# Performance work log

Hardware: AMD Instinct MI355X
Metric: run time of the kernel (lower is better)

The kernel has to match this reference:

```python
import jax, jax.numpy as jnp
import numpy as np

T = 64      # simulation_length
B = 128     # batch
D = 2048    # flattened input dim / axons per core
N = 2048    # neurons per core
L = 4       # number of cores (chain, latency = index)
OUT = 1024  # number of output_sources


def setup_inputs() -> dict:
    key = jax.random.key(0)
    k0, k1, k2, k3 = jax.random.split(key, 4)
    x = jax.random.uniform(k0, (B, D), dtype=jnp.float32)          # rate-coded input in [0,1)
    # core_params[l] = core_matrix.transpose() -> shape [N, A]; scaled for sane membrane dynamics
    W = jax.random.normal(k1, (L, N, D), dtype=jnp.float32) * 0.05
    thresholds = jnp.ones((L,), dtype=jnp.float32)
    # axon_sources: per-core irregular gather indices into previous core's neurons (input for l=0)
    axon_idx = jax.random.randint(k2, (L, D), 0, D, dtype=jnp.int32)
    out_idx = jax.random.randint(k3, (OUT,), 0, N, dtype=jnp.int32)
    return dict(x=x, W=W, thresholds=thresholds, axon_idx=axon_idx,
                out_idx=out_idx, simulation_length=T)


def _ideal_spike_scan(avg, thr, T):
    """Per-cycle: m += avg; spike = (m > thr); m[m > thr] -= thr.  avg: [B, N]."""
    def step(m, _):
        m = m + avg
        s = (m > thr).astype(m.dtype)
        return m - thr * s, s
    _, spikes = jax.lax.scan(step, jnp.zeros_like(avg), None, length=T)
    return spikes  # [T, B, N]


def reference(x, W, thresholds, axon_idx, out_idx, simulation_length):
    T = simulation_length
    L = W.shape[0]
    # generate_input_spike_train: x replicated across all cycles -> cache[-1]
    prev = jnp.broadcast_to(x, (T,) + x.shape)  # [T, B, D]
    for l in range(L):
        # get_signal_tensor: gather axon source signals for every cycle
        gathered = prev[:, :, axon_idx[l]]                    # [T, B, A]
        # per-cycle matmul: torch.matmul(core_params, sig.T).T == sig @ W[l].T
        val = jnp.einsum('tba,na->tbn', gathered, W[l])       # [T, B, N]
        avg = val.mean(axis=0)                                # avg_values [B, N]
        # ideal membrane integrate + threshold-reset recurrence -> out spike train
        prev = _ideal_spike_scan(avg, thresholds[l], T)       # [T, B, N]
    # output_signals: sum of output-source spikes over all cycles
    return prev[:, :, out_idx].sum(axis=0)                    # [B, OUT]
```

## Files before the change

kernel.cpp:

```cpp
#include <hip/hip_runtime.h>

#define BB   128
#define DD   2048
#define NN   2048
#define LL   4
#define OUTN 1024
#define JBQ  32

typedef double double4v __attribute__((ext_vector_type(4)));

__global__ __launch_bounds__(256) void gather0_kernel(
    const float* __restrict__ x, const int* __restrict__ idx0,
    float* __restrict__ At)
{
    int i = blockIdx.x * 256 + threadIdx.x;
    int k = i >> 7;
    int b = i & 127;
    At[i] = x[b * DD + idx0[k]];
}

__global__ __launch_bounds__(256, 2) void layer_kernel(
    const float* __restrict__ srcT,
    const int*   __restrict__ idx,
    const float* __restrict__ Wl,
    const float* __restrict__ thresholds, int l,
    const int*   __restrict__ Tptr,
    float* __restrict__ dst, int isLast)
{
    __shared__ double red[4 * 64 * 8];

    const int t    = threadIdx.x;
    const int wq   = t >> 6;
    const int lane = t & 63;
    const int q    = lane >> 4;
    const int c    = lane & 15;

    const int g     = blockIdx.x;
    const int btile = (g >> 3) & 7;
    const int nsup  = (g & 7) | ((g >> 6) << 3);
    const int n0    = nsup * 32;
    const int bcol  = btile * 16 + c;

    double4v pr = {0., 0., 0., 0.}, pcv = {0., 0., 0., 0.};
    pr  = __builtin_amdgcn_mfma_f64_16x16x4f64(0.25 * (double)c, 1.0, pr, 0, 0, 0);
    pcv = __builtin_amdgcn_mfma_f64_16x16x4f64(0.25, (double)c, pcv, 0, 0, 0);
    int rowD[4], colD[4];
    #pragma unroll
    for (int r = 0; r < 4; ++r) {
        rowD[r] = (int)(pr[r] + 0.25);
        colD[r] = (int)(pcv[r] + 0.25);
    }

    double4v acc0[4] = {{0.,0.,0.,0.},{0.,0.,0.,0.},{0.,0.,0.,0.},{0.,0.,0.,0.}};
    double4v acc1[4] = {{0.,0.,0.,0.},{0.,0.,0.,0.},{0.,0.,0.,0.},{0.,0.,0.,0.}};

    const int    kbase = wq * (DD / 4);
    const float* wb0   = Wl + (size_t)(n0 + c) * DD + kbase + 4 * q;
    const float* wb1   = wb0 + (size_t)16 * DD;
    const int*   ibase = idx ? (idx + kbase + 4 * q) : nullptr;

    float4 wv0[4], wv1[4];
    float4 sv[4];
    int4   iv[4];

    #pragma unroll
    for (int p = 0; p < 4; ++p) {
        wv0[p] = *(const float4*)(wb0 + 16 * p);
        wv1[p] = *(const float4*)(wb1 + 16 * p);
    }
    #pragma unroll
    for (int p = 0; p < 4; ++p) {
        int r0, r1, r2, r3;
        if (ibase) {
            int4 iv0 = *(const int4*)(ibase + 16 * p);
            r0 = iv0.x; r1 = iv0.y; r2 = iv0.z; r3 = iv0.w;
        } else {
            int kb = kbase + 16 * p + 4 * q;
            r0 = kb; r1 = kb + 1; r2 = kb + 2; r3 = kb + 3;
        }
        sv[p].x = srcT[(size_t)r0 * BB + bcol];
        sv[p].y = srcT[(size_t)r1 * BB + bcol];
        sv[p].z = srcT[(size_t)r2 * BB + bcol];
        sv[p].w = srcT[(size_t)r3 * BB + bcol];
    }
    if (ibase) {
        #pragma unroll
        for (int p = 0; p < 4; ++p) iv[p] = *(const int4*)(ibase + 16 * (4 + p));
    }

    for (int u = 0; u < JBQ / 4; ++u) {
        #pragma unroll
        for (int gg = 0; gg < 4; ++gg) {
            float4 w0 = wv0[gg];
            float4 w1 = wv1[gg];
            float4 s  = sv[gg];

            int jn = 4 * u + 4 + gg; if (jn > JBQ - 1) jn = JBQ - 1;
            wv0[gg] = *(const float4*)(wb0 + 16 * jn);
            wv1[gg] = *(const float4*)(wb1 + 16 * jn);

            int r0, r1, r2, r3;
            if (ibase) {
                int4 ivv = iv[gg];
                r0 = ivv.x; r1 = ivv.y; r2 = ivv.z; r3 = ivv.w;
            } else {
                int kb = kbase + 16 * jn + 4 * q;
                r0 = kb; r1 = kb + 1; r2 = kb + 2; r3 = kb + 3;
            }
            sv[gg].x = srcT[(size_t)r0 * BB + bcol];
            sv[gg].y = srcT[(size_t)r1 * BB + bcol];
            sv[gg].z = srcT[(size_t)r2 * BB + bcol];
            sv[gg].w = srcT[(size_t)r3 * BB + bcol];

            if (ibase) {
                int jm = 4 * u + 8 + gg; if (jm > JBQ - 1) jm = JBQ - 1;
                iv[gg] = *(const int4*)(ibase + 16 * jm);
            }

            acc0[0] = __builtin_amdgcn_mfma_f64_16x16x4f64((double)w0.x, (double)s.x, acc0[0], 0, 0, 0);
            acc1[0] = __builtin_amdgcn_mfma_f64_16x16x4f64((double)w1.x, (double)s.x, acc1[0], 0, 0, 0);
            acc0[1] = __builtin_amdgcn_mfma_f64_16x16x4f64((double)w0.y, (double)s.y, acc0[1], 0, 0, 0);
            acc1[1] = __builtin_amdgcn_mfma_f64_16x16x4f64((double)w1.y, (double)s.y, acc1[1], 0, 0, 0);
            acc0[2] = __builtin_amdgcn_mfma_f64_16x16x4f64((double)w0.z, (double)s.z, acc0[2], 0, 0, 0);
            acc1[2] = __builtin_amdgcn_mfma_f64_16x16x4f64((double)w1.z, (double)s.z, acc1[2], 0, 0, 0);
            acc0[3] = __builtin_amdgcn_mfma_f64_16x16x4f64((double)w0.w, (double)s.w, acc0[3], 0, 0, 0);
            acc1[3] = __builtin_amdgcn_mfma_f64_16x16x4f64((double)w1.w, (double)s.w, acc1[3], 0, 0, 0);
        }
    }

    double4v a0 = (acc0[0] + acc0[1]) + (acc0[2] + acc0[3]);
    double4v a1 = (acc1[0] + acc1[1]) + (acc1[2] + acc1[3]);

    {
        double* my = red + ((size_t)wq * 64 + lane) * 8;
        #pragma unroll
        for (int r = 0; r < 4; ++r) { my[r] = a0[r]; my[4 + r] = a1[r]; }
    }
    __syncthreads();
    if (wq < 2) {
        const int off = wq * 4;
        double a[4];
        #pragma unroll
        for (int r = 0; r < 4; ++r) {
            a[r] =  red[((size_t)0 * 64 + lane) * 8 + off + r];
            a[r] += red[((size_t)1 * 64 + lane) * 8 + off + r];
            a[r] += red[((size_t)2 * 64 + lane) * 8 + off + r];
            a[r] += red[((size_t)3 * 64 + lane) * 8 + off + r];
        }

        const double th = (double)thresholds[l];
        const int T = *Tptr;
        const float sc = isLast ? 1.0f : (1.0f / (float)T);
        double m0 = 0., m1 = 0., m2 = 0., m3 = 0.;
        int c0 = 0, c1 = 0, c2 = 0, c3 = 0;
        for (int tt = 0; tt < T; ++tt) {
            m0 += a[0]; if (m0 > th) { c0++; m0 -= th; }
            m1 += a[1]; if (m1 > th) { c1++; m1 -= th; }
            m2 += a[2]; if (m2 > th) { c2++; m2 -= th; }
            m3 += a[3]; if (m3 > th) { c3++; m3 -= th; }
        }
        int cnt[4] = {c0, c1, c2, c3};
        #pragma unroll
        for (int r = 0; r < 4; ++r) {
            int n = n0 + 16 * wq + rowD[r];
            dst[(size_t)n * BB + btile * 16 + colD[r]] = (float)cnt[r] * sc;
        }
    }
}

__global__ __launch_bounds__(256) void out_kernel(
    const float* __restrict__ cntT, const int* __restrict__ out_idx,
    float* __restrict__ out)
{
    int i = blockIdx.x * 256 + threadIdx.x;
    int b = i >> 10;
    int o = i & 1023;
    out[i] = cntT[(size_t)out_idx[o] * BB + b];
}

extern "C" void kernel_launch(void* const* d_in, const int* in_sizes, int n_in,
                              void* d_out, int out_size, void* d_ws, size_t ws_size,
                              hipStream_t stream)
{
    const float* x    = (const float*)d_in[0];
    const float* W    = (const float*)d_in[1];
    const float* thr  = (const float*)d_in[2];
    const int*   axon = (const int*)d_in[3];
    const int*   oidx = (const int*)d_in[4];
    const int*   Tptr = (const int*)d_in[5];
    float* out = (float*)d_out;

    char* ws = (char*)d_ws;
    float* At   = (float*)ws;
    float* mA   = (float*)(ws + (1u << 20));
    float* mB   = (float*)(ws + (2u << 20));
    float* cntT = (float*)(ws + (3u << 20));

    gather0_kernel<<<(DD * BB) / 256, 256, 0, stream>>>(x, axon, At);

    const float* srcs[LL] = { At, mA, mB, mA };
    float*       dsts[LL] = { mA, mB, mA, cntT };
    for (int l = 0; l < LL; ++l) {
        const int* idx = (l == 0) ? nullptr : (axon + (size_t)l * DD);
        layer_kernel<<<512, 256, 0, stream>>>(
            srcs[l], idx, W + (size_t)l * NN * DD, thr, l, Tptr,
            dsts[l], (l == LL - 1) ? 1 : 0);
    }

    out_kernel<<<(BB * OUTN) / 256, 256, 0, stream>>>(cntT, oidx, out);
}
```

Baseline: 227.2 us.

## Use exact int8 multi-digit MFMA for spike-count layers instead of FP64

For layers 1-3 the input is an integer spike count (0..T), so W is split into seven 7-bit digits of a 48-bit fixed-point value and the matmul runs on int8 MFMA, reconstructed exactly in double with an offset correction. Each call adds a per-layer weight digitisation kernel and an int8 gather kernel, and layer kernels also emit int8 counts. The aim is to replace slow FP64 MFMA with much higher-throughput int8 MFMA. The cost is extra passes writing about 7 bytes per weight element each call, plus a dependence on workspace size being large enough.

```diff
diff --git a/kernel.cpp b/kernel.cpp
--- a/kernel.cpp
+++ b/kernel.cpp
@@ -6,8 +6,11 @@
 #define LL   4
 #define OUTN 1024
 #define JBQ  32
+#define NDIG 7
 
 typedef double double4v __attribute__((ext_vector_type(4)));
+typedef int    int4v    __attribute__((ext_vector_type(4)));
+typedef char   char4v   __attribute__((ext_vector_type(4)));
 
 __global__ __launch_bounds__(256) void gather0_kernel(
     const float* __restrict__ x, const int* __restrict__ idx0,
@@ -17,6 +20,39 @@
     int k = i >> 7;
     int b = i & 127;
     At[i] = x[b * DD + idx0[k]];
+}
+
+__global__ __launch_bounds__(256) void wdig7_kernel(
+    const float* __restrict__ Wl, signed char* __restrict__ Wd)
+{
+    const size_t DP = (size_t)NN * DD;
+    size_t i  = (size_t)blockIdx.x * 256 + threadIdx.x;
+    size_t r4 = i * 4;
+    float4 w = *(const float4*)(Wl + r4);
+    const float wv[4] = {w.x, w.y, w.z, w.w};
+    unsigned long long V[4];
+    #pragma unroll
+    for (int e = 0; e < 4; ++e)
+        V[e] = (unsigned long long)(__double2ll_rn((double)wv[e] * 0x1p48)
+                                    + (1LL << 47));
+    #pragma unroll
+    for (int j = 0; j < NDIG; ++j) {
+        char4v p = { (char)((V[0] >> (7 * j)) & 127),
+                     (char)((V[1] >> (7 * j)) & 127),
+                     (char)((V[2] >> (7 * j)) & 127),
+                     (char)((V[3] >> (7 * j)) & 127) };
+        *(char4v*)(Wd + (size_t)j * DP + r4) = p;
+    }
+}
+
+__global__ __launch_bounds__(256) void gather8_kernel(
+    const signed char* __restrict__ c8T, const int* __restrict__ idx,
+    signed char* __restrict__ g8T)
+{
+    int i = blockIdx.x * 256 + threadIdx.x;
+    int b = i >> 11;
+    int k = i & (DD - 1);
+    g8T[i] = c8T[(size_t)b * DD + idx[k]];
 }
 
 __global__ __launch_bounds__(256, 2) void layer_kernel(
@@ -25,7 +61,7 @@
     const float* __restrict__ Wl,
     const float* __restrict__ thresholds, int l,
     const int*   __restrict__ Tptr,
-    float* __restrict__ dst, int isLast)
+    float* __restrict__ dst, signed char* __restrict__ c8T, int isLast)
 {
     __shared__ double red[4 * 64 * 8];
 
@@ -163,7 +199,127 @@
         #pragma unroll
         for (int r = 0; r < 4; ++r) {
             int n = n0 + 16 * wq + rowD[r];
-            dst[(size_t)n * BB + btile * 16 + colD[r]] = (float)cnt[r] * sc;
+            int b = btile * 16 + colD[r];
+            dst[(size_t)n * BB + b] = (float)cnt[r] * sc;
+            if (c8T) c8T[(size_t)b * NN + n] = (signed char)cnt[r];
+        }
+    }
+}
+
+__global__ __launch_bounds__(256, 2) void layer_i8_kernel(
+    const signed char* __restrict__ B8,
+    const signed char* __restrict__ Wd7,
+    const float* __restrict__ thresholds, int l,
+    const int*   __restrict__ Tptr,
+    float* __restrict__ dst, signed char* __restrict__ c8T, int isLast)
+{
+    __shared__ double red[4 * 64 * 8];
+
+    const int t    = threadIdx.x;
+    const int wq   = t >> 6;
+    const int lane = t & 63;
+    const int q    = lane >> 4;
+    const int c    = lane & 15;
+
+    const int g     = blockIdx.x;
+    const int btile = (g >> 3) & 7;
+    const int nsup  = (g & 7) | ((g >> 6) << 3);
+    const int n0    = nsup * 32;
+    const int bcol  = btile * 16 + c;
+
+    int rowD[4], colD[4];
+    {
+        const int cb  = c * 0x01010101;
+        const int hot = (q == 0) ? 1 : 0;
+        int4v aLab = {cb, cb, cb, cb};
+        int4v oneh = {hot, 0, 0, 0};
+        int4v dR = {0, 0, 0, 0}, dC = {0, 0, 0, 0};
+        dR = __builtin_amdgcn_mfma_i32_16x16x64_i8(aLab, oneh, dR, 0, 0, 0);
+        dC = __builtin_amdgcn_mfma_i32_16x16x64_i8(oneh, aLab, dC, 0, 0, 0);
+        #pragma unroll
+        for (int r = 0; r < 4; ++r) { rowD[r] = dR[r]; colD[r] = dC[r]; }
+    }
+
+    int4v acc0[NDIG], acc1[NDIG], accS = (int4v)0;
+    #pragma unroll
+    for (int j = 0; j < NDIG; ++j) { acc0[j] = (int4v)0; acc1[j] = (int4v)0; }
+
+    const size_t DP = (size_t)NN * DD;
+    const int kbase = wq * (DD / 4);
+    const signed char* ap0 = Wd7 + (size_t)(n0 + c) * DD + kbase + 16 * q;
+    const signed char* ap1 = ap0 + (size_t)16 * DD;
+    const signed char* bp  = B8  + (size_t)bcol * DD + kbase + 16 * q;
+
+    const int4v ones = {0x01010101, 0x01010101, 0x01010101, 0x01010101};
+
+    #pragma unroll
+    for (int kc = 0; kc < 8; ++kc) {
+        const int off = kc * 64;
+        int4v bfv = *(const int4v*)(bp + off);
+        int4v a0[NDIG], a1[NDIG];
+        #pragma unroll
+        for (int j = 0; j < NDIG; ++j) {
+            a0[j] = *(const int4v*)(ap0 + (size_t)j * DP + off);
+            a1[j] = *(const int4v*)(ap1 + (size_t)j * DP + off);
+        }
+        #pragma unroll
+        for (int j = 0; j < NDIG; ++j) {
+            acc0[j] = __builtin_amdgcn_mfma_i32_16x16x64_i8(a0[j], bfv, acc0[j], 0, 0, 0);
+            acc1[j] = __builtin_amdgcn_mfma_i32_16x16x64_i8(a1[j], bfv, acc1[j], 0, 0, 0);
+        }
+        accS = __builtin_amdgcn_mfma_i32_16x16x64_i8(ones, bfv, accS, 0, 0, 0);
+    }
+
+    const double S0 = 0x1p-48, S1 = 0x1p-41, S2 = 0x1p-34, S3 = 0x1p-27,
+                 S4 = 0x1p-20, S5 = 0x1p-13, S6 = 0x1p-6;
+    {
+        double* my = red + ((size_t)wq * 64 + lane) * 8;
+        #pragma unroll
+        for (int r = 0; r < 4; ++r) {
+            double corr = 0.5 * (double)accS[r];
+            my[r]     = S0 * (double)acc0[0][r] + S1 * (double)acc0[1][r]
+                      + S2 * (double)acc0[2][r] + S3 * (double)acc0[3][r]
+                      + S4 * (double)acc0[4][r] + S5 * (double)acc0[5][r]
+                      + S6 * (double)acc0[6][r] - corr;
+            my[4 + r] = S0 * (double)acc1[0][r] + S1 * (double)acc1[1][r]
+                      + S2 * (double)acc1[2][r] + S3 * (double)acc1[3][r]
+                      + S4 * (double)acc1[4][r] + S5 * (double)acc1[5][r]
+                      + S6 * (double)acc1[6][r] - corr;
+        }
+    }
+    __syncthreads();
+    if (wq < 2) {
+        const int off = wq * 4;
+        double a[4];
+        #pragma unroll
+        for (int r = 0; r < 4; ++r) {
+            a[r] =  red[((size_t)0 * 64 + lane) * 8 + off + r];
+            a[r] += red[((size_t)1 * 64 + lane) * 8 + off + r];
+            a[r] += red[((size_t)2 * 64 + lane) * 8 + off + r];
+            a[r] += red[((size_t)3 * 64 + lane) * 8 + off + r];
+        }
+
+        const double th = (double)thresholds[l];
+        const int T = *Tptr;
+        const double invT = 1.0 / (double)T;
+        const float sc = isLast ? 1.0f : (1.0f / (float)T);
+        double m0 = 0., m1 = 0., m2 = 0., m3 = 0.;
+        int c0 = 0, c1 = 0, c2 = 0, c3 = 0;
+        const double v0 = a[0] * invT, v1 = a[1] * invT,
+                     v2 = a[2] * invT, v3 = a[3] * invT;
+        for (int tt = 0; tt < T; ++tt) {
+            m0 += v0; if (m0 > th) { c0++; m0 -= th; }
+            m1 += v1; if (m1 > th) { c1++; m1 -= th; }
+            m2 += v2; if (m2 > th) { c2++; m2 -= th; }
+            m3 += v3; if (m3 > th) { c3++; m3 -= th; }
+        }
+        int cnt[4] = {c0, c1, c2, c3};
+        #pragma unroll
+        for (int r = 0; r < 4; ++r) {
+            int n = n0 + 16 * wq + rowD[r];
+            int b = btile * 16 + colD[r];
+            dst[(size_t)n * BB + b] = (float)cnt[r] * sc;
+            if (c8T) c8T[(size_t)b * NN + n] = (signed char)cnt[r];
         }
     }
 }
@@ -190,21 +346,46 @@
     const int*   Tptr = (const int*)d_in[5];
     float* out = (float*)d_out;
 
+    const size_t DP = (size_t)NN * DD;
     char* ws = (char*)d_ws;
     float* At   = (float*)ws;
     float* mA   = (float*)(ws + (1u << 20));
     float* mB   = (float*)(ws + (2u << 20));
     float* cntT = (float*)(ws + (3u << 20));
+    signed char* c8A = (signed char*)(ws + (4u << 20));
+    signed char* c8B = (signed char*)(ws + (4u << 20) + (256u << 10));
+    signed char* g8T = (signed char*)(ws + (4u << 20) + (512u << 10));
+    signed char* Wd  = (signed char*)(ws + (5u << 20));
+
+    const int useI8 = (ws_size >= ((size_t)34 << 20)) ? 1 : 0;
 
     gather0_kernel<<<(DD * BB) / 256, 256, 0, stream>>>(x, axon, At);
 
-    const float* srcs[LL] = { At, mA, mB, mA };
-    float*       dsts[LL] = { mA, mB, mA, cntT };
-    for (int l = 0; l < LL; ++l) {
-        const int* idx = (l == 0) ? nullptr : (axon + (size_t)l * DD);
+    if (!useI8) {
+        const float* srcs[LL] = { At, mA, mB, mA };
+        float*       dsts[LL] = { mA, mB, mA, cntT };
+        for (int l = 0; l < LL; ++l) {
+            const int* idx = (l == 0) ? nullptr : (axon + (size_t)l * DD);
+            layer_kernel<<<512, 256, 0, stream>>>(
+                srcs[l], idx, W + (size_t)l * NN * DD, thr, l, Tptr,
+                dsts[l], nullptr, (l == LL - 1) ? 1 : 0);
+        }
+    } else {
         layer_kernel<<<512, 256, 0, stream>>>(
-            srcs[l], idx, W + (size_t)l * NN * DD, thr, l, Tptr,
-            dsts[l], (l == LL - 1) ? 1 : 0);
+            At, nullptr, W, thr, 0, Tptr, mA, c8A, 0);
+
+        signed char* c8s[3] = { c8A, c8B, c8A };
+        signed char* c8d[3] = { c8B, c8A, nullptr };
+        float*       fds[3] = { mB, mA, cntT };
+        for (int l = 1; l < LL; ++l) {
+            wdig7_kernel<<<(int)(DP / 4) / 256, 256, 0, stream>>>(
+                W + (size_t)l * DP, Wd);
+            gather8_kernel<<<(BB * DD) / 256, 256, 0, stream>>>(
+                c8s[l - 1], axon + (size_t)l * DD, g8T);
+            layer_i8_kernel<<<512, 256, 0, stream>>>(
+                g8T, Wd, thr, l, Tptr, fds[l - 1], c8d[l - 1],
+                (l == LL - 1) ? 1 : 0);
+        }
     }
 
     out_kernel<<<(BB * OUTN) / 256, 256, 0, stream>>>(cntT, oidx, out);
```

Measured after the change: 267.6 us. 1.18x slower.
